# Performance work log

Measured on AMD Instinct MI355X. Metric: run time of the kernel, lower is better.

The kernel has to match this reference:

```python
import jax, jax.numpy as jnp
import numpy as np

N = 10000
E = 256000
MUL = 32            # multiplicity per l (hidden_sizes = [32]*4)
NB = 10             # nbasis_funcs
RMAX = 3.5          # max_radius
NAVG = 25.6         # navg_neighbors
NGRAPH = 16         # number of graphs in batch
SLICES = [(0, 1), (1, 4), (4, 9), (9, 16)]  # l=0..3 blocks of the 16-dim SH rep


def _sph_harm(u):
    """Real spherical harmonics l=0..3, component normalization, on unit vectors. [E,16]"""
    x, y, z = u[:, 0], u[:, 1], u[:, 2]
    one = jnp.ones_like(x)
    s3 = 3.0 ** 0.5
    s15 = 15.0 ** 0.5
    s5 = 5.0 ** 0.5
    a = (35.0 / 8.0) ** 0.5
    b = 105.0 ** 0.5
    c = (21.0 / 8.0) ** 0.5
    d = 7.0 ** 0.5 / 2.0
    cols = [
        one,
        s3 * x, s3 * y, s3 * z,
        s15 * x * y, s15 * y * z, 0.5 * s5 * (3 * z * z - 1), s15 * x * z, 0.5 * s15 * (x * x - y * y),
        a * y * (3 * x * x - y * y), b * x * y * z, c * y * (5 * z * z - 1), d * z * (5 * z * z - 3),
        c * x * (5 * z * z - 1), 0.5 * b * z * (x * x - y * y), a * x * (x * x - 3 * y * y),
    ]
    return jnp.stack(cols, axis=1)


def _radial(emb, W1, W2):
    # FullyConnectedNet-style MLP with fan-in normalization and silu
    h = jax.nn.silu(emb @ W1 / (NB ** 0.5))
    return h @ W2 / (W1.shape[1] ** 0.5)


def _edge_geometry(pos, edge_src, edge_dst):
    vec = pos[edge_src] - pos[edge_dst]          # [E,3]
    r = jnp.linalg.norm(vec, axis=1)             # [E]
    u = vec / (r[:, None] + 1e-9)
    sh = _sph_harm(u)                            # [E,16]
    t = jnp.clip(r / RMAX, 0.0, 1.0)
    cutoff = jnp.where(r < RMAX, 0.5 * (jnp.cos(jnp.pi * t) + 1.0), 0.0)
    edge_attr = cutoff[:, None] * sh             # [E,16]
    centers = jnp.linspace(0.0, RMAX, NB)
    step = RMAX / (NB - 1)
    emb = jnp.exp(-(((r[:, None] - centers) / step) ** 2)) / 1.12 * (NB ** 0.5)
    return edge_attr, emb


def _layer(feat, edge_src, edge_dst, edge_attr, emb, Wsc, Wr1, Wr2):
    """Gated interaction block: self-connection + per-edge radial-weighted TP conv + gate."""
    n = feat.shape[0]
    # self-connection: per-l channel mixing
    sc = jnp.concatenate(
        [jnp.einsum('nci,co->noi', feat[:, :, a:b], Wsc[l]) for l, (a, b) in enumerate(SLICES)],
        axis=2) / (MUL ** 0.5)
    # per-edge weights from radial MLP: [E, 2 paths, 4 l's, MUL]
    w = _radial(emb, Wr1, Wr2).reshape(-1, 2, 4, MUL)
    xs = feat[edge_src]                          # [E,MUL,16] gather
    # path A (0e x Yl -> l) for l=0, plus path B (l x Yl -> 0e) for l=1..3 -> scalar slot
    scal = w[:, 0, 0, :] * xs[:, :, 0] * edge_attr[:, 0:1]
    parts = []
    for l, (a, b) in enumerate(SLICES):
        if l == 0:
            continue
        scal = scal + w[:, 1, l, :] * jnp.einsum('eci,ei->ec', xs[:, :, a:b], edge_attr[:, a:b])
        parts.append(w[:, 0, l, :, None] * xs[:, :, 0:1] * edge_attr[:, None, a:b])
    msg = jnp.concatenate([scal[:, :, None]] + parts, axis=2)   # [E,MUL,16]
    agg = jax.ops.segment_sum(msg, edge_dst, num_segments=n) / (NAVG ** 0.5)
    y = sc + agg
    # equivariant gate: silu on scalars, sigmoid(scalar) gates l>0 features
    s = y[:, :, 0]
    return jnp.concatenate(
        [jax.nn.silu(s)[:, :, None], y[:, :, 1:] * jax.nn.sigmoid(s)[:, :, None]], axis=2)


def _forward(pos, x, batch, edge_src, edge_dst, W_sc, Wr1, Wr2, Wf1, Wf2):
    n = pos.shape[0]
    edge_attr, emb = _edge_geometry(pos, edge_src, edge_dst)
    # lift scalar input features into the full l=0..3 layout
    feat = jnp.zeros((n, MUL, 16), x.dtype).at[:, :, 0].set(x)
    for i in range(3):
        feat = _layer(feat, edge_src, edge_dst, edge_attr, emb, W_sc[i], Wr1[i], Wr2[i])
    # final interaction block -> 1x0e output per node
    wf = _radial(emb, Wf1, Wf2).reshape(-1, 4, MUL)             # [E,4,MUL]
    xs = feat[edge_src]
    ms = wf[:, 0, :] * xs[:, :, 0] * edge_attr[:, 0:1]
    for l, (a, b) in enumerate(SLICES):
        if l == 0:
            continue
        ms = ms + wf[:, l, :] * jnp.einsum('eci,ei->ec', xs[:, :, a:b], edge_attr[:, a:b])
    node = jax.ops.segment_sum(ms.sum(axis=1) / (MUL ** 0.5), edge_dst, num_segments=n) / (NAVG ** 0.5)
    out = jax.ops.segment_sum(node, batch, num_segments=NGRAPH) / (NAVG ** 0.5)
    return out.flatten()


def setup_inputs() -> dict:
    key = jax.random.key(0)
    ks = jax.random.split(key, 10)
    pos = jax.random.uniform(ks[0], (N, 3), jnp.float32) * 5.0
    x = jax.random.normal(ks[1], (N, MUL), jnp.float32)
    batch = jnp.sort(jax.random.randint(ks[2], (N,), 0, NGRAPH, jnp.int32))
    edge_src = jax.random.randint(ks[3], (E,), 0, N, jnp.int32)
    edge_dst = jax.random.randint(ks[4], (E,), 0, N, jnp.int32)
    W_sc = jax.random.normal(ks[5], (3, 4, MUL, MUL), jnp.float32)
    Wr1 = jax.random.normal(ks[6], (3, NB, 64), jnp.float32)
    Wr2 = jax.random.normal(ks[7], (3, 64, 2 * 4 * MUL), jnp.float32)
    Wf1 = jax.random.normal(ks[8], (NB, 64), jnp.float32)
    Wf2 = jax.random.normal(ks[9], (64, 4 * MUL), jnp.float32)
    return {"pos": pos, "x": x, "batch": batch, "edge_src": edge_src, "edge_dst": edge_dst,
            "W_sc": W_sc, "Wr1": Wr1, "Wr2": Wr2, "Wf1": Wf1, "Wf2": Wf2}


def reference(pos, x, batch, edge_src, edge_dst, W_sc, Wr1, Wr2, Wf1, Wf2):
    return _forward(pos, x, batch, edge_src, edge_dst, W_sc, Wr1, Wr2, Wf1, Wf2)
```

## Files before the change

kernel.cpp:

```cpp
#include <hip/hip_runtime.h>
#include <math.h>

#define NN 10000
#define EE 256000
#define NGR 16
#define ECAP 150016

#define RSQRT10F   0.31622776601683794f
#define EMB_SCALE  2.8234621965789103f
#define INV_SQRT_MUL  0.17677669529663687f
#define INV_SQRT_NAVG 0.19764235376052372f
#define SCREC      (0.125f * INV_SQRT_NAVG)
#define STEPF      0.3888888888888889f
#define INV_STEPF  2.5714285714285716f
#define PIF        3.14159265358979323846f

__device__ __forceinline__ float sigm(float x) {
    return 1.0f / (1.0f + __expf(-x));
}

__device__ __forceinline__ void atomAddF(float* p, float v) {
    __hip_atomic_fetch_add(p, v, __ATOMIC_RELAXED, __HIP_MEMORY_SCOPE_AGENT);
}

__global__ __launch_bounds__(256) void count_kernel(
    const float* __restrict__ pos, const int* __restrict__ esrc,
    const int* __restrict__ edst, int* __restrict__ deg)
{
    int e = blockIdx.x * 256 + threadIdx.x;
    if (e >= EE) return;
    int s = esrc[e], d = edst[e];
    float vx = pos[3*s+0] - pos[3*d+0];
    float vy = pos[3*s+1] - pos[3*d+1];
    float vz = pos[3*s+2] - pos[3*d+2];
    float r2 = vx*vx + vy*vy + vz*vz;
    if (r2 < 12.25f) atomicAdd(&deg[d], 1);
}

__global__ __launch_bounds__(256) void scan_kernel(
    const int* __restrict__ deg, int* __restrict__ off, int* __restrict__ cursor)
{
    __shared__ int sbuf[256];
    const int t = threadIdx.x;
    const int start = t * 40;
    const int end = (start + 40 < NN) ? start + 40 : NN;
    int s = 0;
    for (int i = start; i < end; ++i) s += deg[i];
    sbuf[t] = s;
    __syncthreads();
    for (int d = 1; d < 256; d <<= 1) {
        int v = (t >= d) ? sbuf[t - d] : 0;
        __syncthreads();
        sbuf[t] += v;
        __syncthreads();
    }
    int run = sbuf[t] - s;
    for (int i = start; i < end; ++i) {
        off[i] = run; cursor[i] = run; run += deg[i];
    }
    if (t == 255) off[NN] = sbuf[255];
}

__global__ __launch_bounds__(256) void w1t_kernel(
    const float* __restrict__ Wr1, const float* __restrict__ Wf1,
    float* __restrict__ w1t)
{
    int t = blockIdx.x * 256 + threadIdx.x;
    if (t >= 4096) return;
    int i = t & 15;
    int j = (t >> 4) & 63;
    int l = t >> 10;
    float v;
    if (l < 3) v = (i < 10) ? Wr1[l * 640 + i * 64 + j] : 0.0f;
    else       v = (i < 10) ? Wf1[i * 64 + j] : 0.0f;
    w1t[l * 1024 + j * 16 + i] = v;
}

__global__ __launch_bounds__(256) void pack_kernel(
    const float* __restrict__ Wr2, const float* __restrict__ Wf2,
    float* __restrict__ wr2p, float* __restrict__ wf2p)
{
    const int offs[7] = {0, 32, 64, 96, 160, 192, 224};
    int t = blockIdx.x * 256 + threadIdx.x;
    if (t < 49152) {
        int k = t & 63;
        int j = (t >> 6) & 63;
        int g = (t >> 12) & 3;
        int layer = t >> 14;
        float v = 0.0f;
        if (k < 56)
            v = Wr2[layer * 16384 + j * 256 + offs[k >> 3] + g * 8 + (k & 7)];
        wr2p[t] = v;
    } else if (t < 49152 + 8192) {
        int t2 = t - 49152;
        int u = t2 & 15;
        int l = (t2 >> 4) & 3;
        int j = (t2 >> 6) & 63;
        int g = t2 >> 12;
        wf2p[t2] = Wf2[j * 128 + l * 32 + g * 16 + u];
    }
}

__global__ __launch_bounds__(256) void scatter_kernel(
    const float* __restrict__ pos, const int* __restrict__ esrc,
    const int* __restrict__ edst, int* __restrict__ cursor,
    int* __restrict__ csrc, int* __restrict__ cdst,
    float* __restrict__ attr_soa, float* __restrict__ attr_e,
    float* __restrict__ emb_soa)
{
    int e = blockIdx.x * 256 + threadIdx.x;
    if (e >= EE) return;
    int s = esrc[e], d = edst[e];
    float vx = pos[3*s+0] - pos[3*d+0];
    float vy = pos[3*s+1] - pos[3*d+1];
    float vz = pos[3*s+2] - pos[3*d+2];
    float r2 = vx*vx + vy*vy + vz*vz;
    if (r2 >= 12.25f) return;
    float r = sqrtf(r2);
    int slot = atomicAdd(&cursor[d], 1);
    if (slot >= ECAP) return;

    float inv = 1.0f / (r + 1e-9f);
    float x = vx * inv, y = vy * inv, z = vz * inv;

    float t = r * (1.0f / 3.5f);
    float cw = 0.5f * (cosf(PIF * t) + 1.0f);

    const float s3  = 1.7320508075688772f;
    const float s15 = 3.872983346207417f;
    const float s5  = 2.23606797749979f;
    const float a4  = 2.0916500663351889f;
    const float b4  = 10.246950765959598f;
    const float c4  = 1.6201851746019651f;
    const float d4  = 1.3228756555322954f;
    float xx = x*x, yy = y*y, zz = z*z;
    float sh[16];
    sh[0]  = 1.0f;
    sh[1]  = s3 * x;
    sh[2]  = s3 * y;
    sh[3]  = s3 * z;
    sh[4]  = s15 * x * y;
    sh[5]  = s15 * y * z;
    sh[6]  = 0.5f * s5 * (3.0f*zz - 1.0f);
    sh[7]  = s15 * x * z;
    sh[8]  = 0.5f * s15 * (xx - yy);
    sh[9]  = a4 * y * (3.0f*xx - yy);
    sh[10] = b4 * x * y * z;
    sh[11] = c4 * y * (5.0f*zz - 1.0f);
    sh[12] = d4 * z * (5.0f*zz - 3.0f);
    sh[13] = c4 * x * (5.0f*zz - 1.0f);
    sh[14] = 0.5f * b4 * z * (xx - yy);
    sh[15] = a4 * x * (xx - 3.0f*yy);

    float4* ae = (float4*)(attr_e + (size_t)slot * 16);
    #pragma unroll
    for (int q = 0; q < 4; ++q)
        ae[q] = make_float4(cw*sh[q*4], cw*sh[q*4+1], cw*sh[q*4+2], cw*sh[q*4+3]);

    #pragma unroll
    for (int i = 0; i < 16; ++i)
        attr_soa[(size_t)i * ECAP + slot] = cw * sh[i];
    #pragma unroll
    for (int k = 0; k < 10; ++k) {
        float dd = (r - (float)k * STEPF) * INV_STEPF;
        emb_soa[(size_t)k * ECAP + slot] = __expf(-dd * dd) * EMB_SCALE;
    }
    csrc[slot] = s;
    cdst[slot] = d;
}

__global__ __launch_bounds__(256) void init_feat_kernel(
    const float* __restrict__ x, float* __restrict__ feat)
{
    int t = blockIdx.x * 256 + threadIdx.x;
    if (t >= NN * 512) return;
    int i = t & 15;
    int c = (t >> 4) & 31;
    int n = t >> 9;
    feat[t] = (i == 0) ? x[n * 32 + c] : 0.0f;
}

__global__ __launch_bounds__(256) void h_kernel(
    const float* __restrict__ w1t, const float* __restrict__ emb_soa,
    float* __restrict__ h_soa, const int* __restrict__ cntp)
{
    const int tid = threadIdx.x;
    int cnt = *cntp; if (cnt > ECAP) cnt = ECAP;
    if (cnt == 0) return;
    const int e = blockIdx.x * 256 + tid;
    if (blockIdx.x * 256 >= cnt) return;
    const bool alive = (e < cnt);
    const int ee = alive ? e : (cnt - 1);

    float emb[10];
    #pragma unroll
    for (int i = 0; i < 10; ++i)
        emb[i] = emb_soa[(size_t)i * ECAP + ee];

    #pragma unroll 4
    for (int j = 0; j < 64; ++j) {
        const float* wj = w1t + j * 16;
        float a = 0.0f;
        #pragma unroll
        for (int i = 0; i < 10; ++i)
            a += emb[i] * wj[i];
        a *= RSQRT10F;
        if (alive)
            h_soa[(size_t)j * ECAP + e] = a * sigm(a);
    }
}

__global__ __launch_bounds__(256, 4) void edge_mlp_kernel(
    const float* __restrict__ wr2p, const float* __restrict__ h_soa,
    const float* __restrict__ fin, float* __restrict__ rec,
    const int* __restrict__ csrc,
    const float* __restrict__ attr_soa, const int* __restrict__ cntp)
{
    const int tid = threadIdx.x;
    const int g = blockIdx.y;
    const int c0 = g * 8;
    int cnt = *cntp; if (cnt > ECAP) cnt = ECAP;
    if (cnt == 0) return;
    const int e = blockIdx.x * 256 + tid;
    if (blockIdx.x * 256 >= cnt) return;
    const bool alive = (e < cnt);
    const int ee = alive ? e : (cnt - 1);

    float attr[16];
    #pragma unroll
    for (int i = 0; i < 16; ++i)
        attr[i] = attr_soa[(size_t)i * ECAP + ee];

    const float* xb = fin + (size_t)csrc[ee] * 512;
    const float* hp = h_soa + ee;
    const float* wg = wr2p + (size_t)g * 4096;
    float4* rec4 = (float4*)rec;

    float a0[8], a1[8], a2[8], a3[8], a4[8], a5[8], a6[8];
    #pragma unroll
    for (int u = 0; u < 8; ++u) {
        a0[u] = 0.f; a1[u] = 0.f; a2[u] = 0.f; a3[u] = 0.f;
        a4[u] = 0.f; a5[u] = 0.f; a6[u] = 0.f;
    }
    #pragma unroll 4
    for (int j = 0; j < 64; ++j) {
        const float hj = hp[(size_t)j * ECAP];
        const float* w = wg + j * 64;
        #pragma unroll
        for (int u = 0; u < 8; ++u) {
            a0[u] += hj * w[u];
            a1[u] += hj * w[8 + u];
            a2[u] += hj * w[16 + u];
            a3[u] += hj * w[24 + u];
            a4[u] += hj * w[32 + u];
            a5[u] += hj * w[40 + u];
            a6[u] += hj * w[48 + u];
        }
    }
    #pragma unroll
    for (int u = 0; u < 8; ++u) {
        const int c = c0 + u;
        const float4* xv = (const float4*)(xb + c * 16);
        float4 x0 = xv[0], x1 = xv[1], x2 = xv[2], x3 = xv[3];
        float d1 = x0.y*attr[1] + x0.z*attr[2] + x0.w*attr[3];
        float d2 = x1.x*attr[4] + x1.y*attr[5] + x1.z*attr[6]
                 + x1.w*attr[7] + x2.x*attr[8];
        float d3 = x2.y*attr[9] + x2.z*attr[10] + x2.w*attr[11]
                 + x3.x*attr[12] + x3.y*attr[13] + x3.z*attr[14]
                 + x3.w*attr[15];
        const float xs0 = x0.x;
        float scal = SCREC * (a0[u]*xs0*attr[0] + a4[u]*d1 + a5[u]*d2 + a6[u]*d3);
        float px = SCREC * xs0;
        if (alive)
            rec4[(size_t)c * ECAP + e] =
                make_float4(scal, a1[u] * px, a2[u] * px, a3[u] * px);
    }
}

__global__ __launch_bounds__(256) void agg_kernel(
    const float* __restrict__ fin, float* __restrict__ fout,
    const float* __restrict__ Wsc, const float* __restrict__ rec,
    const float* __restrict__ attr_e, const int* __restrict__ off)
{
    int t = blockIdx.x * 256 + threadIdx.x;
    int c = t & 31;
    int n = t >> 5;
    if (n >= NN) return;

    float acc[16];
    #pragma unroll
    for (int i = 0; i < 16; ++i) acc[i] = 0.0f;

    const float* f = fin + (size_t)n * 512;
    for (int cin = 0; cin < 32; ++cin) {
        float w0 = Wsc[          cin * 32 + c];
        float w1 = Wsc[1024 + cin * 32 + c];
        float w2 = Wsc[2048 + cin * 32 + c];
        float w3 = Wsc[3072 + cin * 32 + c];
        const float4* fv = (const float4*)(f + cin * 16);
        float4 f0 = fv[0], f1 = fv[1], f2 = fv[2], f3 = fv[3];
        acc[0]  += f0.x * w0;
        acc[1]  += f0.y * w1; acc[2]  += f0.z * w1; acc[3]  += f0.w * w1;
        acc[4]  += f1.x * w2; acc[5]  += f1.y * w2; acc[6]  += f1.z * w2;
        acc[7]  += f1.w * w2; acc[8]  += f2.x * w2;
        acc[9]  += f2.y * w3; acc[10] += f2.z * w3; acc[11] += f2.w * w3;
        acc[12] += f3.x * w3; acc[13] += f3.y * w3; acc[14] += f3.z * w3;
        acc[15] += f3.w * w3;
    }
    #pragma unroll
    for (int i = 0; i < 16; ++i) acc[i] *= INV_SQRT_MUL;

    const float4* rec4 = (const float4*)rec;
    int e0 = off[n], e1 = off[n + 1];
    if (e1 > ECAP) e1 = ECAP;
    for (int e = e0; e < e1; ++e) {
        float4 v = rec4[(size_t)c * ECAP + e];
        const float4* av = (const float4*)(attr_e + (size_t)e * 16);
        float4 A0 = av[0], A1 = av[1], A2 = av[2], A3 = av[3];
        acc[0]  += v.x;
        acc[1]  += v.y * A0.y;
        acc[2]  += v.y * A0.z;
        acc[3]  += v.y * A0.w;
        acc[4]  += v.z * A1.x;
        acc[5]  += v.z * A1.y;
        acc[6]  += v.z * A1.z;
        acc[7]  += v.z * A1.w;
        acc[8]  += v.z * A2.x;
        acc[9]  += v.w * A2.y;
        acc[10] += v.w * A2.z;
        acc[11] += v.w * A2.w;
        acc[12] += v.w * A3.x;
        acc[13] += v.w * A3.y;
        acc[14] += v.w * A3.z;
        acc[15] += v.w * A3.w;
    }

    float s = acc[0];
    float g = sigm(s);
    float4 o0 = make_float4(s * g,      acc[1] * g,  acc[2] * g,  acc[3] * g);
    float4 o1 = make_float4(acc[4] * g, acc[5] * g,  acc[6] * g,  acc[7] * g);
    float4 o2 = make_float4(acc[8] * g, acc[9] * g,  acc[10] * g, acc[11] * g);
    float4 o3 = make_float4(acc[12] * g, acc[13] * g, acc[14] * g, acc[15] * g);
    float4* ov = (float4*)(fout + (size_t)n * 512 + c * 16);
    ov[0] = o0; ov[1] = o1; ov[2] = o2; ov[3] = o3;
}

__global__ __launch_bounds__(256, 4) void final_edge_kernel(
    const float* __restrict__ wf2p, const float* __restrict__ h_soa,
    const float* __restrict__ fin, float* __restrict__ fbuf,
    const int* __restrict__ csrc,
    const float* __restrict__ attr_soa, const int* __restrict__ cntp)
{
    const int tid = threadIdx.x;
    const int g = blockIdx.y;
    const int c0 = g * 16;
    int cnt = *cntp; if (cnt > ECAP) cnt = ECAP;
    if (cnt == 0) return;
    const int e = blockIdx.x * 256 + tid;
    if (blockIdx.x * 256 >= cnt) return;
    const bool alive = (e < cnt);
    const int ee = alive ? e : (cnt - 1);

    float attr[16];
    #pragma unroll
    for (int i = 0; i < 16; ++i)
        attr[i] = attr_soa[(size_t)i * ECAP + ee];

    const float* xb = fin + (size_t)csrc[ee] * 512;
    float d0[16], d1[16], d2[16], d3[16];
    #pragma unroll
    for (int u = 0; u < 16; ++u) {
        const float4* xv = (const float4*)(xb + (c0 + u) * 16);
        float4 x0 = xv[0], x1 = xv[1], x2 = xv[2], x3 = xv[3];
        d0[u] = x0.x * attr[0];
        d1[u] = x0.y*attr[1] + x0.z*attr[2] + x0.w*attr[3];
        d2[u] = x1.x*attr[4] + x1.y*attr[5] + x1.z*attr[6]
              + x1.w*attr[7] + x2.x*attr[8];
        d3[u] = x2.y*attr[9] + x2.z*attr[10] + x2.w*attr[11]
              + x3.x*attr[12] + x3.y*attr[13] + x3.z*attr[14]
              + x3.w*attr[15];
    }

    const float* hp = h_soa + ee;
    const float* wg = wf2p + (size_t)g * 4096;
    float acc0 = 0.f, acc1 = 0.f, acc2 = 0.f, acc3 = 0.f;
    #pragma unroll 2
    for (int j = 0; j < 64; ++j) {
        const float hj = hp[(size_t)j * ECAP];
        const float* w = wg + j * 64;
        float t0 = 0.f, t1 = 0.f, t2 = 0.f, t3 = 0.f;
        #pragma unroll
        for (int u = 0; u < 16; ++u) {
            t0 += d0[u] * w[u];
            t1 += d1[u] * w[16 + u];
            t2 += d2[u] * w[32 + u];
            t3 += d3[u] * w[48 + u];
        }
        acc0 += hj * t0; acc1 += hj * t1;
        acc2 += hj * t2; acc3 += hj * t3;
    }
    if (alive)
        fbuf[(size_t)g * ECAP + e] = (acc0 + acc1 + acc2 + acc3) * 0.125f;
}

__global__ __launch_bounds__(256) void out_kernel(
    const float* __restrict__ fbuf, const int* __restrict__ off,
    const int* __restrict__ batch, float* __restrict__ out)
{
    __shared__ float bins[NGR];
    int t = blockIdx.x * 256 + threadIdx.x;
    if (threadIdx.x < NGR) bins[threadIdx.x] = 0.0f;
    __syncthreads();
    if (t < NN) {
        int e0 = off[t], e1 = off[t + 1];
        if (e1 > ECAP) e1 = ECAP;
        float s = 0.0f;
        for (int e = e0; e < e1; ++e)
            s += fbuf[e] + fbuf[(size_t)ECAP + e];
        atomicAdd(&bins[batch[t]], s * (INV_SQRT_MUL * (1.0f / 25.6f)));
    }
    __syncthreads();
    if (threadIdx.x < NGR) atomAddF(out + threadIdx.x, bins[threadIdx.x]);
}

extern "C" void kernel_launch(void* const* d_in, const int* in_sizes, int n_in,
                              void* d_out, int out_size, void* d_ws, size_t ws_size,
                              hipStream_t stream)
{
    const float* pos  = (const float*)d_in[0];
    const float* x    = (const float*)d_in[1];
    const int*   batch= (const int*)  d_in[2];
    const int*   esrc = (const int*)  d_in[3];
    const int*   edst = (const int*)  d_in[4];
    const float* W_sc = (const float*)d_in[5];
    const float* Wr1  = (const float*)d_in[6];
    const float* Wr2  = (const float*)d_in[7];
    const float* Wf1  = (const float*)d_in[8];
    const float* Wf2  = (const float*)d_in[9];
    float* out = (float*)d_out;

    char* ws = (char*)d_ws;
    size_t off_b = 0;
    auto alloc = [&](size_t bytes) -> void* {
        void* p = ws + off_b;
        off_b = (off_b + bytes + 255) & ~(size_t)255;
        return p;
    };
    int*   deg      = (int*)  alloc((size_t)NN * 4);
    int*   off      = (int*)  alloc((size_t)(NN + 1) * 4);
    int*   cursor   = (int*)  alloc((size_t)NN * 4);
    int*   csrc     = (int*)  alloc((size_t)ECAP * 4);
    int*   cdst     = (int*)  alloc((size_t)ECAP * 4);
    float* w1t      = (float*)alloc((size_t)4 * 1024 * 4);
    float* wr2p     = (float*)alloc((size_t)3 * 16384 * 4);
    float* wf2p     = (float*)alloc((size_t)8192 * 4);
    float* emb_soa  = (float*)alloc((size_t)10 * ECAP * 4);
    float* attr_soa = (float*)alloc((size_t)16 * ECAP * 4);
    float* attr_e   = (float*)alloc((size_t)16 * ECAP * 4);
    float* h_soa    = (float*)alloc((size_t)64 * ECAP * 4);
    float* rec      = (float*)alloc((size_t)128 * ECAP * 4);
    float* feat_a   = (float*)alloc((size_t)NN * 512 * 4);
    float* feat_b   = (float*)alloc((size_t)NN * 512 * 4);

    hipMemsetAsync(deg, 0, (size_t)NN * 4, stream);
    hipMemsetAsync(d_out, 0, (size_t)out_size * 4, stream);

    count_kernel<<<(EE + 255) / 256, 256, 0, stream>>>(pos, esrc, edst, deg);
    scan_kernel<<<1, 256, 0, stream>>>(deg, off, cursor);
    w1t_kernel<<<16, 256, 0, stream>>>(Wr1, Wf1, w1t);
    pack_kernel<<<(49152 + 8192 + 255) / 256, 256, 0, stream>>>(
        Wr2, Wf2, wr2p, wf2p);
    scatter_kernel<<<(EE + 255) / 256, 256, 0, stream>>>(
        pos, esrc, edst, cursor, csrc, cdst, attr_soa, attr_e, emb_soa);
    init_feat_kernel<<<(NN * 512 + 255) / 256, 256, 0, stream>>>(x, feat_a);

    const int* cntp = off + NN;
    float* fin = feat_a;
    float* fout = feat_b;
    dim3 egrid(ECAP / 256, 4);
    for (int layer = 0; layer < 3; ++layer) {
        h_kernel<<<ECAP / 256, 256, 0, stream>>>(
            w1t + layer * 1024, emb_soa, h_soa, cntp);
        edge_mlp_kernel<<<egrid, 256, 0, stream>>>(
            wr2p + (size_t)layer * 16384, h_soa, fin, rec,
            csrc, attr_soa, cntp);
        agg_kernel<<<(NN * 32 + 255) / 256, 256, 0, stream>>>(
            fin, fout, W_sc + layer * 4096, rec, attr_e, off);
        float* tmp = fin; fin = fout; fout = tmp;
    }
    h_kernel<<<ECAP / 256, 256, 0, stream>>>(
        w1t + 3 * 1024, emb_soa, h_soa, cntp);
    float* fbuf = rec;
    final_edge_kernel<<<dim3(ECAP / 256, 2), 256, 0, stream>>>(
        wf2p, h_soa, fin, fbuf, csrc, attr_soa, cntp);
    out_kernel<<<(NN + 255) / 256, 256, 0, stream>>>(fbuf, off, batch, out);
}
```

Measured before the change: 879.6 us.

## Stage gathered source features through LDS and reorder final edge contraction

In the final edge kernel, the radial weights are first contracted with the hidden activations into per-channel coefficients (H0..H3). The source-node feature gather is then done cooperatively, with four threads per edge loading one 64-byte channel row as float4 into LDS, followed by the dot with attr. This aims to turn per-thread strided 256-byte gathers into more coalesced wavefront loads. The cost is 16 block-wide barriers, about 21 KB of LDS per block, and 64 live accumulators per thread, all of which may reduce occupancy.

Result: slower. 987.6 us (+12.3%).

```diff
diff --git a/kernel.cpp b/kernel.cpp
--- a/kernel.cpp
+++ b/kernel.cpp
@@ -351,6 +351,9 @@
     const int* __restrict__ csrc,
     const float* __restrict__ attr_soa, const int* __restrict__ cntp)
 {
+    __shared__ int   lds_src[256];
+    __shared__ float lds_x[256 * 20];
+
     const int tid = threadIdx.x;
     const int g = blockIdx.y;
     const int c0 = g * 16;
@@ -361,46 +364,62 @@
     const bool alive = (e < cnt);
     const int ee = alive ? e : (cnt - 1);
 
+    lds_src[tid] = csrc[ee];
+
     float attr[16];
     #pragma unroll
     for (int i = 0; i < 16; ++i)
         attr[i] = attr_soa[(size_t)i * ECAP + ee];
 
-    const float* xb = fin + (size_t)csrc[ee] * 512;
-    float d0[16], d1[16], d2[16], d3[16];
-    #pragma unroll
-    for (int u = 0; u < 16; ++u) {
-        const float4* xv = (const float4*)(xb + (c0 + u) * 16);
-        float4 x0 = xv[0], x1 = xv[1], x2 = xv[2], x3 = xv[3];
-        d0[u] = x0.x * attr[0];
-        d1[u] = x0.y*attr[1] + x0.z*attr[2] + x0.w*attr[3];
-        d2[u] = x1.x*attr[4] + x1.y*attr[5] + x1.z*attr[6]
-              + x1.w*attr[7] + x2.x*attr[8];
-        d3[u] = x2.y*attr[9] + x2.z*attr[10] + x2.w*attr[11]
-              + x3.x*attr[12] + x3.y*attr[13] + x3.z*attr[14]
-              + x3.w*attr[15];
-    }
-
     const float* hp = h_soa + ee;
     const float* wg = wf2p + (size_t)g * 4096;
-    float acc0 = 0.f, acc1 = 0.f, acc2 = 0.f, acc3 = 0.f;
+    float H0[16], H1[16], H2[16], H3[16];
+    #pragma unroll
+    for (int u = 0; u < 16; ++u) { H0[u]=0.f; H1[u]=0.f; H2[u]=0.f; H3[u]=0.f; }
     #pragma unroll 2
     for (int j = 0; j < 64; ++j) {
         const float hj = hp[(size_t)j * ECAP];
         const float* w = wg + j * 64;
-        float t0 = 0.f, t1 = 0.f, t2 = 0.f, t3 = 0.f;
         #pragma unroll
         for (int u = 0; u < 16; ++u) {
-            t0 += d0[u] * w[u];
-            t1 += d1[u] * w[16 + u];
-            t2 += d2[u] * w[32 + u];
-            t3 += d3[u] * w[48 + u];
+            H0[u] += hj * w[u];
+            H1[u] += hj * w[16 + u];
+            H2[u] += hj * w[32 + u];
+            H3[u] += hj * w[48 + u];
         }
-        acc0 += hj * t0; acc1 += hj * t1;
-        acc2 += hj * t2; acc3 += hj * t3;
-    }
+    }
+
+    __syncthreads();
+
+    float msum = 0.0f;
+    #pragma unroll
+    for (int u = 0; u < 16; ++u) {
+        const int c = c0 + u;
+        #pragma unroll
+        for (int q = 0; q < 4; ++q) {
+            const int el = q * 64 + (tid >> 2);
+            const int part = tid & 3;
+            const int src = lds_src[el];
+            const float4 v = *(const float4*)(fin + (size_t)src * 512
+                                              + c * 16 + part * 4);
+            *(float4*)(&lds_x[el * 20 + part * 4]) = v;
+        }
+        __syncthreads();
+        const float4* xr = (const float4*)(&lds_x[tid * 20]);
+        float4 x0 = xr[0], x1 = xr[1], x2 = xr[2], x3 = xr[3];
+        float d0 = x0.x * attr[0];
+        float d1 = x0.y*attr[1] + x0.z*attr[2] + x0.w*attr[3];
+        float d2 = x1.x*attr[4] + x1.y*attr[5] + x1.z*attr[6]
+                 + x1.w*attr[7] + x2.x*attr[8];
+        float d3 = x2.y*attr[9] + x2.z*attr[10] + x2.w*attr[11]
+                 + x3.x*attr[12] + x3.y*attr[13] + x3.z*attr[14]
+                 + x3.w*attr[15];
+        msum += H0[u]*d0 + H1[u]*d1 + H2[u]*d2 + H3[u]*d3;
+        __syncthreads();
+    }
+
     if (alive)
-        fbuf[(size_t)g * ECAP + e] = (acc0 + acc1 + acc2 + acc3) * 0.125f;
+        fbuf[(size_t)g * ECAP + e] = msum * 0.125f;
 }
 
 __global__ __launch_bounds__(256) void out_kernel(
```
